# Performance work log

Measured on AMD Instinct MI355X. Metric: run time of the kernel, lower is better.

## Reference

```python
import jax, jax.numpy as jnp
import numpy as np

EPS = 1e-6
TEMPERATURE = 0.75
SINKHORN_ITERS = 7
BUCKETS = 128


def setup_inputs() -> dict:
    key = jax.random.key(0)
    k1, k2, k3, k4, k5 = jax.random.split(key, 5)
    b, h, t, dh = 2, 8, 8192, 128
    q = jax.random.normal(k1, (b, h, t, dh), dtype=jnp.float32)
    k = jax.random.normal(k2, (b, h, t, dh), dtype=jnp.float32)
    v = jax.random.normal(k3, (b, h, t, dh), dtype=jnp.float32)
    # SimpleSortNet linear: (1, heads, 2*dim_head, buckets)
    W_sort = jax.random.normal(k4, (1, h, 2 * dh, BUCKETS), dtype=jnp.float32)
    # uniform noise used to build gumbel samples (torch samples internally)
    u_gumbel = jax.random.uniform(k5, (b * h, BUCKETS, BUCKETS), dtype=jnp.float32)
    return {"q": q, "k": k, "v": v, "W_sort": W_sort, "u_gumbel": u_gumbel}


def _gumbel_sinkhorn(R, u):
    # R >= 0 (post-relu). r = (log(R+eps) + gumbel) / temperature
    g = -jnp.log(-jnp.log(u + EPS) + EPS)
    r = (jnp.log(R + EPS) + g) / TEMPERATURE
    for _ in range(SINKHORN_ITERS):
        r = r - jax.nn.logsumexp(r, axis=2, keepdims=True)
        r = r - jax.nn.logsumexp(r, axis=1, keepdims=True)
    return jnp.exp(r)


def reference(q, k, v, W_sort, u_gumbel):
    b, h, t, dh = q.shape
    dim = h * dh  # full model dim, used for the softmax scale (matches torch)
    bh = b * h
    buckets = W_sort.shape[-1]
    bsz = t // buckets

    qm = q.reshape(bh, t, dh)
    km = k.reshape(bh, t, dh)
    vm = v.reshape(bh, t, dh)

    b_q = qm.reshape(bh, buckets, bsz, dh)
    b_k = km.reshape(bh, buckets, bsz, dh)
    b_v = vm.reshape(bh, buckets, bsz, dh)

    # SimpleSortNet: per-bucket sums of q and k -> linear -> relu
    x = jnp.concatenate([b_q.sum(axis=2), b_k.sum(axis=2)], axis=-1)  # (bh, buckets, 2*dh)
    W = jnp.broadcast_to(W_sort, (b, h, 2 * dh, buckets)).reshape(bh, 2 * dh, buckets)
    R = jax.nn.relu(jnp.einsum('bue,bek->buk', x, W))  # (bh, buckets, buckets)

    R = _gumbel_sinkhorn(R, u_gumbel)

    # zero_all_but_top along dim=2 with k=1 (keep argmax entry per row)
    idx = jnp.argmax(R, axis=2, keepdims=True)  # (bh, buckets, 1)
    mask = jnp.arange(buckets)[None, None, :] == idx
    R = jnp.where(mask, R, 0.0)

    # reorder buckets: butd = sum_v R[buv] * b_k[bvtd]
    b_k_r = jnp.einsum('buv,bvtd->butd', R, b_k)
    b_v_r = jnp.einsum('buv,bvtd->butd', R, b_v)

    b_k_cat = jnp.concatenate([b_k_r, b_k], axis=2)  # (bh, buckets, 2*bsz, dh)
    b_v_cat = jnp.concatenate([b_v_r, b_v], axis=2)

    dots = jnp.einsum('buie,buje->buij', b_q, b_k_cat) * (dim ** -0.5)
    attn = jax.nn.softmax(dots, axis=-1)
    out = jnp.einsum('buij,buje->buie', attn, b_v_cat)  # (bh, buckets, bsz, dh)

    return out.reshape(b, h, t, dh)
```

## Files before the change

kernel.cpp:

```cpp
#include <hip/hip_runtime.h>
#include <hip/hip_bf16.h>

#define T_SEQ   8192
#define DH      128
#define NBH     16
#define NBUCK   128
#define BSZ     64
#define EPSF    1e-6f

#define SWZ(r)  (((((r) & 7) ^ (((r) >> 3) & 7))) << 3)
#define CF4(v,c) ((c)==0 ? (v).x : (c)==1 ? (v).y : (c)==2 ? (v).z : (v).w)
#define CU4(v,c) ((c)==0 ? (v).x : (c)==1 ? (v).y : (c)==2 ? (v).z : (v).w)

typedef __attribute__((ext_vector_type(8))) __bf16 bf16x8;
typedef __attribute__((ext_vector_type(4))) float  f32x4;

static __device__ __forceinline__ unsigned short f2bf(float f) {
  __bf16 h = (__bf16)f;
  return __builtin_bit_cast(unsigned short, h);
}

__global__ __launch_bounds__(256) void k_bsort(
    const float* __restrict__ q, const float* __restrict__ k,
    const float* __restrict__ W, const float* __restrict__ ug,
    float* __restrict__ rbuf) {
  const int u = blockIdx.x, bh = blockIdx.y;
  const int t = threadIdx.x;
  const int c4g = t & 31;
  const int grp = t >> 5;

  __shared__ float4 xrq[8][32];
  __shared__ float4 xrk[8][32];
  __shared__ float  x[256];
  __shared__ float  part[256];

  {
    const size_t base = ((size_t)bh * T_SEQ + (size_t)u * BSZ + grp * 8) * DH + c4g * 4;
    float4 aq = {0.f, 0.f, 0.f, 0.f};
    float4 ak = {0.f, 0.f, 0.f, 0.f};
    #pragma unroll
    for (int r = 0; r < 8; r++) {
      float4 vq = *(const float4*)(q + base + (size_t)r * DH);
      float4 vk = *(const float4*)(k + base + (size_t)r * DH);
      aq.x += vq.x; aq.y += vq.y; aq.z += vq.z; aq.w += vq.w;
      ak.x += vk.x; ak.y += vk.y; ak.z += vk.z; ak.w += vk.w;
    }
    xrq[grp][c4g] = aq;
    xrk[grp][c4g] = ak;
  }
  __syncthreads();
  if (t < 64) {
    const int which = t >> 5;
    const int cg = t & 31;
    float4 s4 = which ? xrk[0][cg] : xrq[0][cg];
    #pragma unroll
    for (int j = 1; j < 8; j++) {
      float4 o = which ? xrk[j][cg] : xrq[j][cg];
      s4.x += o.x; s4.y += o.y; s4.z += o.z; s4.w += o.w;
    }
    *(float4*)(&x[which * 128 + cg * 4]) = s4;
  }
  __syncthreads();
  {
    const int eh = t >> 7;
    const int vcol = t & 127;
    const float* Wp = W + ((size_t)(bh & 7) * 256 + (size_t)eh * 128) * NBUCK + vcol;
    float racc = 0.f;
    #pragma unroll 16
    for (int e = 0; e < 128; e++) racc += x[eh * 128 + e] * Wp[(size_t)e * NBUCK];
    part[t] = racc;
  }
  __syncthreads();
  if (t < 128) {
    float R = part[t] + part[t + 128];
    R = fmaxf(R, 0.f) + EPSF;
    float gu = ug[((size_t)bh * NBUCK + u) * NBUCK + t] + EPSF;
    float g = -logf(-logf(gu) + EPSF);
    rbuf[((size_t)bh * NBUCK + u) * NBUCK + t] = (logf(R) + g) * (1.f / 0.75f);
  }
}

__global__ __launch_bounds__(512, 1) void k_sinkhorn(
    const float* __restrict__ rbuf, int* __restrict__ idxb, float* __restrict__ sb) {
  const int bh = blockIdx.x;
  const int t  = threadIdx.x;
  const int own = t >> 2;
  const int qq  = t & 3;
  __shared__ float rl[128 * 129];
  __shared__ float ca[128], ra[128];

  const float* rb = rbuf + (size_t)bh * (NBUCK * NBUCK);
  for (int i = t; i < NBUCK * NBUCK; i += 512)
    rl[(i >> 7) * 129 + (i & 127)] = rb[i];
  if (t < 128) ca[t] = 0.f;
  __syncthreads();

  float rowv[32], colv[32];
  #pragma unroll
  for (int i4 = 0; i4 < 8; i4++) {
    float4 vv = *(const float4*)(&rl[own * 129 + qq * 32 + i4 * 4]);
    rowv[i4 * 4 + 0] = vv.x; rowv[i4 * 4 + 1] = vv.y;
    rowv[i4 * 4 + 2] = vv.z; rowv[i4 * 4 + 3] = vv.w;
  }
  #pragma unroll
  for (int i = 0; i < 32; i++) colv[i] = rl[(qq * 32 + i) * 129 + own];

  for (int iter = 0; iter < 7; iter++) {
    {
      float vals[32];
      float m = -1e30f;
      #pragma unroll
      for (int i4 = 0; i4 < 8; i4++) {
        float4 cc = *(const float4*)(&ca[qq * 32 + i4 * 4]);
        vals[i4 * 4 + 0] = rowv[i4 * 4 + 0] + cc.x;
        vals[i4 * 4 + 1] = rowv[i4 * 4 + 1] + cc.y;
        vals[i4 * 4 + 2] = rowv[i4 * 4 + 2] + cc.z;
        vals[i4 * 4 + 3] = rowv[i4 * 4 + 3] + cc.w;
      }
      #pragma unroll
      for (int i = 0; i < 32; i++) m = fmaxf(m, vals[i]);
      m = fmaxf(m, __shfl_xor(m, 1));
      m = fmaxf(m, __shfl_xor(m, 2));
      float s0 = 0.f, s1 = 0.f, s2 = 0.f, s3 = 0.f;
      #pragma unroll
      for (int i = 0; i < 8; i++) {
        s0 += __expf(vals[i * 4 + 0] - m);
        s1 += __expf(vals[i * 4 + 1] - m);
        s2 += __expf(vals[i * 4 + 2] - m);
        s3 += __expf(vals[i * 4 + 3] - m);
      }
      float ss = (s0 + s1) + (s2 + s3);
      ss += __shfl_xor(ss, 1);
      ss += __shfl_xor(ss, 2);
      if (qq == 0) ra[own] = -(m + logf(ss));
    }
    __syncthreads();
    {
      float vals[32];
      float m = -1e30f;
      #pragma unroll
      for (int i4 = 0; i4 < 8; i4++) {
        float4 rr = *(const float4*)(&ra[qq * 32 + i4 * 4]);
        vals[i4 * 4 + 0] = colv[i4 * 4 + 0] + rr.x;
        vals[i4 * 4 + 1] = colv[i4 * 4 + 1] + rr.y;
        vals[i4 * 4 + 2] = colv[i4 * 4 + 2] + rr.z;
        vals[i4 * 4 + 3] = colv[i4 * 4 + 3] + rr.w;
      }
      #pragma unroll
      for (int i = 0; i < 32; i++) m = fmaxf(m, vals[i]);
      m = fmaxf(m, __shfl_xor(m, 1));
      m = fmaxf(m, __shfl_xor(m, 2));
      float s0 = 0.f, s1 = 0.f, s2 = 0.f, s3 = 0.f;
      #pragma unroll
      for (int i = 0; i < 8; i++) {
        s0 += __expf(vals[i * 4 + 0] - m);
        s1 += __expf(vals[i * 4 + 1] - m);
        s2 += __expf(vals[i * 4 + 2] - m);
        s3 += __expf(vals[i * 4 + 3] - m);
      }
      float ss = (s0 + s1) + (s2 + s3);
      ss += __shfl_xor(ss, 1);
      ss += __shfl_xor(ss, 2);
      if (qq == 0) ca[own] = -(m + logf(ss));
    }
    __syncthreads();
  }

  {
    float best = -1e30f; int bi = qq * 32;
    #pragma unroll
    for (int i = 0; i < 32; i++) {
      float val = rowv[i] + ca[qq * 32 + i];
      if (val > best) { best = val; bi = qq * 32 + i; }
    }
    #pragma unroll
    for (int d = 1; d < 4; d <<= 1) {
      float ob = __shfl_xor(best, d);
      int   oi = __shfl_xor(bi, d);
      if (ob > best || (ob == best && oi < bi)) { best = ob; bi = oi; }
    }
    if (qq == 0) {
      idxb[bh * NBUCK + own] = bi;
      sb[bh * NBUCK + own]   = expf(rl[own * 129 + bi] + ra[own] + ca[bi]);
    }
  }
}

__global__ __launch_bounds__(256) void k_attn(
    const float* __restrict__ q, const float* __restrict__ k, const float* __restrict__ v,
    const int* __restrict__ idxb, const float* __restrict__ sb, float* __restrict__ out) {
  const int bh = blockIdx.x;
  const int u  = blockIdx.y;
  const int t  = threadIdx.x;
  const int lane = t & 63;
  const int w  = t >> 6;
  const int l15 = lane & 15;
  const int lgp = lane >> 4;

  __shared__ uint4 smem4[2048];
  unsigned short* sm = (unsigned short*)smem4;
  #define VBASE 8192

  const int   vidx = idxb[bh * NBUCK + u];
  const float sval = sb[bh * NBUCK + u];
  const size_t hb = (size_t)bh * (T_SEQ * DH);
  const float* qg = q + hb;
  const float* kg = k + hb;
  const float* vg = v + hb;

  const int vj0 = (t >> 4) * 4;
  const int vd0 = (t & 15) * 8;

  #pragma unroll
  for (int it = 0; it < 16; it++) {
    int i = it * 256 + t;
    int row = i >> 5;
    int c4 = (i & 31) << 2;
    int grow = (row < 64) ? (vidx * BSZ + row) : (u * BSZ + (row - 64));
    float4 val = *(const float4*)(kg + (size_t)grow * DH + c4);
    ushort4 hh;
    hh.x = f2bf(val.x); hh.y = f2bf(val.y); hh.z = f2bf(val.z); hh.w = f2bf(val.w);
    *(ushort4*)(sm + (((row * 128 + c4) ^ SWZ(row)))) = hh;
  }
  bf16x8 aQ[4];
  {
    int qrow = u * BSZ + w * 16 + l15;
    const float* qp = qg + (size_t)qrow * DH + lgp * 8;
    #pragma unroll
    for (int kk = 0; kk < 4; kk++) {
      float4 v0 = *(const float4*)(qp + kk * 32);
      float4 v1 = *(const float4*)(qp + kk * 32 + 4);
      bf16x8 f;
      f[0] = (__bf16)v0.x; f[1] = (__bf16)v0.y; f[2] = (__bf16)v0.z; f[3] = (__bf16)v0.w;
      f[4] = (__bf16)v1.x; f[5] = (__bf16)v1.y; f[6] = (__bf16)v1.z; f[7] = (__bf16)v1.w;
      aQ[kk] = f;
    }
  }
  float4 vpre[4][2];
  #pragma unroll
  for (int r = 0; r < 4; r++) {
    const float* vp = vg + (size_t)(vidx * BSZ + vj0 + r) * DH + vd0;
    vpre[r][0] = *(const float4*)(vp);
    vpre[r][1] = *(const float4*)(vp + 4);
  }
  __syncthreads();

  f32x4 accS[8];
  __builtin_amdgcn_s_setprio(1);
  #pragma unroll
  for (int n = 0; n < 8; n++) {
    f32x4 acc = {0.f, 0.f, 0.f, 0.f};
    #pragma unroll
    for (int kk = 0; kk < 4; kk++) {
      int row = n * 16 + l15;
      int c0 = lgp * 8 + kk * 32;
      bf16x8 bK = *(const bf16x8*)(sm + ((row * 128 + c0) ^ SWZ(row)));
      acc = __builtin_amdgcn_mfma_f32_16x16x32_bf16(aQ[kk], bK, acc, 0, 0, 0);
    }
    accS[n] = acc;
  }
  __builtin_amdgcn_s_setprio(0);

  float pval[8][4];
  float lsum[4];
  #pragma unroll
  for (int r = 0; r < 4; r++) {
    float mm = -1e30f;
    #pragma unroll
    for (int n = 0; n < 8; n++) {
      float lg2 = accS[n][r] * 0.03125f * (n < 4 ? sval : 1.0f);
      pval[n][r] = lg2;
      mm = fmaxf(mm, lg2);
    }
    mm = fmaxf(mm, __shfl_xor(mm, 1));
    mm = fmaxf(mm, __shfl_xor(mm, 2));
    mm = fmaxf(mm, __shfl_xor(mm, 4));
    mm = fmaxf(mm, __shfl_xor(mm, 8));
    float ss = 0.f;
    #pragma unroll
    for (int n = 0; n < 8; n++) {
      float p = __expf(pval[n][r] - mm);
      ss += p;
      pval[n][r] = p * (n < 4 ? sval : 1.0f);
    }
    ss += __shfl_xor(ss, 1);
    ss += __shfl_xor(ss, 2);
    ss += __shfl_xor(ss, 4);
    ss += __shfl_xor(ss, 8);
    lsum[r] = ss;
  }

  __syncthreads();

  #pragma unroll
  for (int n = 0; n < 8; n++) {
    #pragma unroll
    for (int r = 0; r < 4; r++) {
      int prow = w * 16 + lgp * 4 + r;
      int pcol = n * 16 + l15;
      sm[(prow * 128 + pcol) ^ SWZ(prow)] = f2bf(pval[n][r]);
    }
  }
  #pragma unroll
  for (int x = 0; x < 8; x++) {
    int d = vd0 + x;
    int h = x >> 2, c = x & 3;
    ushort4 val;
    val.x = f2bf(CF4(vpre[0][h], c));
    val.y = f2bf(CF4(vpre[1][h], c));
    val.z = f2bf(CF4(vpre[2][h], c));
    val.w = f2bf(CF4(vpre[3][h], c));
    *(ushort4*)(sm + VBASE + d * 64 + (vj0 ^ SWZ(d))) = val;
  }
  ushort4 v2p[4][2];
  #pragma unroll
  for (int r = 0; r < 4; r++) {
    const float* vp = vg + (size_t)(u * BSZ + vj0 + r) * DH + vd0;
    #pragma unroll
    for (int h = 0; h < 2; h++) {
      float4 ld = *(const float4*)(vp + h * 4);
      v2p[r][h].x = f2bf(ld.x); v2p[r][h].y = f2bf(ld.y);
      v2p[r][h].z = f2bf(ld.z); v2p[r][h].w = f2bf(ld.w);
    }
  }
  __syncthreads();

  bf16x8 aP[4];
  #pragma unroll
  for (int kk = 0; kk < 4; kk++) {
    int prow = w * 16 + l15;
    int c0 = lgp * 8 + kk * 32;
    aP[kk] = *(const bf16x8*)(sm + ((prow * 128 + c0) ^ SWZ(prow)));
  }

  f32x4 accO[8];
  __builtin_amdgcn_s_setprio(1);
  #pragma unroll
  for (int n = 0; n < 8; n++) {
    f32x4 acc = {0.f, 0.f, 0.f, 0.f};
    #pragma unroll
    for (int kk = 0; kk < 2; kk++) {
      int d = n * 16 + l15;
      int jj0 = lgp * 8 + kk * 32;
      bf16x8 bV = *(const bf16x8*)(sm + VBASE + d * 64 + (jj0 ^ SWZ(d)));
      acc = __builtin_amdgcn_mfma_f32_16x16x32_bf16(aP[kk], bV, acc, 0, 0, 0);
    }
    accO[n] = acc;
  }
  __builtin_amdgcn_s_setprio(0);
  __syncthreads();

  #pragma unroll
  for (int x = 0; x < 8; x++) {
    int d = vd0 + x;
    int h = x >> 2, c = x & 3;
    ushort4 val;
    val.x = CU4(v2p[0][h], c);
    val.y = CU4(v2p[1][h], c);
    val.z = CU4(v2p[2][h], c);
    val.w = CU4(v2p[3][h], c);
    *(ushort4*)(sm + VBASE + d * 64 + (vj0 ^ SWZ(d))) = val;
  }
  __syncthreads();

  float invl[4];
  #pragma unroll
  for (int r = 0; r < 4; r++) invl[r] = 1.0f / lsum[r];

  __builtin_amdgcn_s_setprio(1);
  #pragma unroll
  for (int n = 0; n < 8; n++) {
    f32x4 acc = accO[n];
    #pragma unroll
    for (int kk = 2; kk < 4; kk++) {
      int d = n * 16 + l15;
      int jj0 = lgp * 8 + (kk - 2) * 32;
      bf16x8 bV = *(const bf16x8*)(sm + VBASE + d * 64 + (jj0 ^ SWZ(d)));
      acc = __builtin_amdgcn_mfma_f32_16x16x32_bf16(aP[kk], bV, acc, 0, 0, 0);
    }
    #pragma unroll
    for (int r = 0; r < 4; r++) {
      int i2 = w * 16 + lgp * 4 + r;
      int d = n * 16 + l15;
      out[((size_t)bh * T_SEQ + (size_t)u * BSZ + i2) * DH + d] = acc[r] * invl[r];
    }
  }
  __builtin_amdgcn_s_setprio(0);
}

extern "C" void kernel_launch(void* const* d_in, const int* in_sizes, int n_in,
                              void* d_out, int out_size, void* d_ws, size_t ws_size,
                              hipStream_t stream) {
  (void)in_sizes; (void)n_in; (void)out_size; (void)ws_size;
  const float* q  = (const float*)d_in[0];
  const float* k  = (const float*)d_in[1];
  const float* v  = (const float*)d_in[2];
  const float* W  = (const float*)d_in[3];
  const float* ug = (const float*)d_in[4];
  float* out = (float*)d_out;

  float* rbuf = (float*)d_ws;
  int*   idxb = (int*)(rbuf + (size_t)NBH * NBUCK * NBUCK);
  float* sb   = (float*)(idxb + NBH * NBUCK);

  k_bsort   <<<dim3(NBUCK, NBH), 256, 0, stream>>>(q, k, W, ug, rbuf);
  k_sinkhorn<<<NBH,              512, 0, stream>>>(rbuf, idxb, sb);
  k_attn    <<<dim3(NBH, NBUCK), 256, 0, stream>>>(q, k, v, idxb, sb, out);
}
```

Measured before the change: 103.8 us.

## Fuse sinkhorn into bucket-sort kernel via last-block atomic counter

```diff
diff --git a/kernel.cpp b/kernel.cpp
--- a/kernel.cpp
+++ b/kernel.cpp
@@ -20,19 +20,26 @@
   return __builtin_bit_cast(unsigned short, h);
 }
 
-__global__ __launch_bounds__(256) void k_bsort(
+__global__ __launch_bounds__(512) void k_bsort(
     const float* __restrict__ q, const float* __restrict__ k,
     const float* __restrict__ W, const float* __restrict__ ug,
-    float* __restrict__ rbuf) {
-  const int u = blockIdx.x, bh = blockIdx.y;
-  const int t = threadIdx.x;
+    float* __restrict__ rbuf, int* __restrict__ idxb, float* __restrict__ sb,
+    int* __restrict__ cnt) {
+  const int th = threadIdx.x;
+  const int sub = th >> 8;
+  const int t  = th & 255;
+  const int u  = blockIdx.x * 2 + sub;
+  const int bh = blockIdx.y;
+
+  __shared__ float4 xrq[2][8][32];
+  __shared__ float4 xrk[2][8][32];
+  __shared__ float  x[2][256];
+  __shared__ float  part[2][256];
+  __shared__ float  ca[128], ra[128];
+  __shared__ int    lastflag;
+
   const int c4g = t & 31;
   const int grp = t >> 5;
-
-  __shared__ float4 xrq[8][32];
-  __shared__ float4 xrk[8][32];
-  __shared__ float  x[256];
-  __shared__ float  part[256];
 
   {
     const size_t base = ((size_t)bh * T_SEQ + (size_t)u * BSZ + grp * 8) * DH + c4g * 4;
@@ -45,20 +52,20 @@
       aq.x += vq.x; aq.y += vq.y; aq.z += vq.z; aq.w += vq.w;
       ak.x += vk.x; ak.y += vk.y; ak.z += vk.z; ak.w += vk.w;
     }
-    xrq[grp][c4g] = aq;
-    xrk[grp][c4g] = ak;
+    xrq[sub][grp][c4g] = aq;
+    xrk[sub][grp][c4g] = ak;
   }
   __syncthreads();
   if (t < 64) {
     const int which = t >> 5;
     const int cg = t & 31;
-    float4 s4 = which ? xrk[0][cg] : xrq[0][cg];
+    float4 s4 = which ? xrk[sub][0][cg] : xrq[sub][0][cg];
     #pragma unroll
     for (int j = 1; j < 8; j++) {
-      float4 o = which ? xrk[j][cg] : xrq[j][cg];
+      float4 o = which ? xrk[sub][j][cg] : xrq[sub][j][cg];
       s4.x += o.x; s4.y += o.y; s4.z += o.z; s4.w += o.w;
     }
-    *(float4*)(&x[which * 128 + cg * 4]) = s4;
+    *(float4*)(&x[sub][which * 128 + cg * 4]) = s4;
   }
   __syncthreads();
   {
@@ -67,43 +74,43 @@
     const float* Wp = W + ((size_t)(bh & 7) * 256 + (size_t)eh * 128) * NBUCK + vcol;
     float racc = 0.f;
     #pragma unroll 16
-    for (int e = 0; e < 128; e++) racc += x[eh * 128 + e] * Wp[(size_t)e * NBUCK];
-    part[t] = racc;
+    for (int e = 0; e < 128; e++) racc += x[sub][eh * 128 + e] * Wp[(size_t)e * NBUCK];
+    part[sub][t] = racc;
   }
   __syncthreads();
   if (t < 128) {
-    float R = part[t] + part[t + 128];
+    float R = part[sub][t] + part[sub][t + 128];
     R = fmaxf(R, 0.f) + EPSF;
     float gu = ug[((size_t)bh * NBUCK + u) * NBUCK + t] + EPSF;
     float g = -logf(-logf(gu) + EPSF);
     rbuf[((size_t)bh * NBUCK + u) * NBUCK + t] = (logf(R) + g) * (1.f / 0.75f);
   }
-}
-
-__global__ __launch_bounds__(512, 1) void k_sinkhorn(
-    const float* __restrict__ rbuf, int* __restrict__ idxb, float* __restrict__ sb) {
-  const int bh = blockIdx.x;
-  const int t  = threadIdx.x;
-  const int own = t >> 2;
-  const int qq  = t & 3;
-  __shared__ float rl[128 * 129];
-  __shared__ float ca[128], ra[128];
-
+
+  __threadfence();
+  __syncthreads();
+  if (th == 0) {
+    int old = atomicAdd(&cnt[bh], 1);
+    lastflag = (old == 63);
+  }
+  __syncthreads();
+  if (!lastflag) return;
+  __threadfence();
+
+  const int own = th >> 2;
+  const int qq  = th & 3;
   const float* rb = rbuf + (size_t)bh * (NBUCK * NBUCK);
-  for (int i = t; i < NBUCK * NBUCK; i += 512)
-    rl[(i >> 7) * 129 + (i & 127)] = rb[i];
-  if (t < 128) ca[t] = 0.f;
-  __syncthreads();
 
   float rowv[32], colv[32];
   #pragma unroll
   for (int i4 = 0; i4 < 8; i4++) {
-    float4 vv = *(const float4*)(&rl[own * 129 + qq * 32 + i4 * 4]);
+    float4 vv = *(const float4*)(rb + own * 128 + qq * 32 + i4 * 4);
     rowv[i4 * 4 + 0] = vv.x; rowv[i4 * 4 + 1] = vv.y;
     rowv[i4 * 4 + 2] = vv.z; rowv[i4 * 4 + 3] = vv.w;
   }
   #pragma unroll
-  for (int i = 0; i < 32; i++) colv[i] = rl[(qq * 32 + i) * 129 + own];
+  for (int i = 0; i < 32; i++) colv[i] = rb[(qq * 32 + i) * 128 + own];
+  if (th < 128) ca[th] = 0.f;
+  __syncthreads();
 
   for (int iter = 0; iter < 7; iter++) {
     {
@@ -181,7 +188,7 @@
     }
     if (qq == 0) {
       idxb[bh * NBUCK + own] = bi;
-      sb[bh * NBUCK + own]   = expf(rl[own * 129 + bi] + ra[own] + ca[bi]);
+      sb[bh * NBUCK + own]   = expf(rb[own * 128 + bi] + ra[own] + ca[bi]);
     }
   }
 }
@@ -402,8 +409,9 @@
   float* rbuf = (float*)d_ws;
   int*   idxb = (int*)(rbuf + (size_t)NBH * NBUCK * NBUCK);
   float* sb   = (float*)(idxb + NBH * NBUCK);
-
-  k_bsort   <<<dim3(NBUCK, NBH), 256, 0, stream>>>(q, k, W, ug, rbuf);
-  k_sinkhorn<<<NBH,              512, 0, stream>>>(rbuf, idxb, sb);
-  k_attn    <<<dim3(NBH, NBUCK), 256, 0, stream>>>(q, k, v, idxb, sb, out);
+  int*   cnt  = (int*)(sb + NBH * NBUCK);
+
+  hipMemsetAsync(cnt, 0, NBH * sizeof(int), stream);
+  k_bsort<<<dim3(64, NBH),   512, 0, stream>>>(q, k, W, ug, rbuf, idxb, sb, cnt);
+  k_attn <<<dim3(NBH, NBUCK), 256, 0, stream>>>(q, k, v, idxb, sb, out);
 }
```

New measurement: 328.2 us. 216% more time.
